# Optimization experiments

Measured on AMD Instinct MI355X. Metric: run time of the kernel, lower is better.

Reference implementation:

```python
import jax, jax.numpy as jnp
import numpy as np

NUM_HEADS = 12
WINDOW = 14  # window size == input_size[0]; rel pos tables are (2*WINDOW-1, head_dim)


def setup_inputs() -> dict:
    key = jax.random.key(0)
    ks = jax.random.split(key, 6)
    C = 768
    x = jax.random.normal(ks[0], (16, 56, 56, C), dtype=jnp.float32)
    qkv_w = jax.random.normal(ks[1], (3 * C, C), dtype=jnp.float32) * 0.02
    qkv_b = jnp.zeros((3 * C,), dtype=jnp.float32)
    proj_w = jax.random.normal(ks[2], (C, C), dtype=jnp.float32) * 0.02
    proj_b = jnp.zeros((C,), dtype=jnp.float32)
    hd = C // NUM_HEADS
    rel_pos_h = jax.random.normal(ks[3], (2 * WINDOW - 1, hd), dtype=jnp.float32) * 0.02
    rel_pos_w = jax.random.normal(ks[4], (2 * WINDOW - 1, hd), dtype=jnp.float32) * 0.02
    return {"x": x, "qkv_w": qkv_w, "qkv_b": qkv_b, "proj_w": proj_w,
            "proj_b": proj_b, "rel_pos_h": rel_pos_h, "rel_pos_w": rel_pos_w}


def reference(x, qkv_w, qkv_b, proj_w, proj_b, rel_pos_h, rel_pos_w):
    B, H, W, C = x.shape
    nh, ws = NUM_HEADS, WINDOW
    hd = C // nh
    scale = hd ** -0.5
    # --- window_partition (H, W divisible by ws -> no padding branch) ---
    xw = x.reshape(B, H // ws, ws, W // ws, ws, C)
    xw = xw.transpose(0, 1, 3, 2, 4, 5).reshape(-1, ws * ws, C)  # (Bw, N, C)
    Bw, N, _ = xw.shape
    # --- qkv projection ---
    qkv = xw @ qkv_w.T + qkv_b  # (Bw, N, 3C)
    qkv = qkv.reshape(Bw, N, 3, nh, hd).transpose(2, 0, 3, 1, 4)
    qkv = qkv.reshape(3, Bw * nh, N, hd)
    q, k, v = qkv[0], qkv[1], qkv[2]
    # --- scaled attention scores ---
    attn = jnp.einsum('bqd,bkd->bqk', q * scale, k)  # (Bw*nh, N, N)
    # --- decomposed relative position bias (q_size == k_size == ws) ---
    idx = jnp.arange(ws)[:, None] - jnp.arange(ws)[None, :] + (ws - 1)
    Rh = rel_pos_h[idx]  # (ws, ws, hd)
    Rw = rel_pos_w[idx]  # (ws, ws, hd)
    rq = q.reshape(Bw * nh, ws, ws, hd)
    rel_h = jnp.einsum('bhwc,hkc->bhwk', rq, Rh)
    rel_w = jnp.einsum('bhwc,wkc->bhwk', rq, Rw)
    attn = (attn.reshape(Bw * nh, ws, ws, ws, ws)
            + rel_h[:, :, :, :, None] + rel_w[:, :, :, None, :])
    attn = jax.nn.softmax(attn.reshape(Bw * nh, N, N), axis=-1)
    # --- weighted values + output projection ---
    out = jnp.einsum('bqk,bkd->bqd', attn, v)
    out = out.reshape(Bw, nh, ws, ws, hd).transpose(0, 2, 3, 1, 4).reshape(Bw, ws, ws, C)
    out = out @ proj_w.T + proj_b
    # --- window_unpartition ---
    out = out.reshape(B, H // ws, W // ws, ws, ws, C)
    out = out.transpose(0, 1, 3, 2, 4, 5).reshape(B, H, W, C)
    return out
```

## Files before the change

kernel.cpp:

```cpp
#include <hip/hip_runtime.h>
#include <stdint.h>

typedef __bf16 bfv8 __attribute__((ext_vector_type(8)));
typedef short s16x8 __attribute__((ext_vector_type(8)));
typedef short s16x4 __attribute__((ext_vector_type(4)));
typedef float f32x4 __attribute__((ext_vector_type(4)));
typedef float f32x16 __attribute__((ext_vector_type(16)));

#define MFMA(a, b, c) __builtin_amdgcn_mfma_f32_16x16x32_bf16(a, b, c, 0, 0, 0)
#define MFMA32(a, b, c) __builtin_amdgcn_mfma_f32_32x32x16_bf16(a, b, c, 0, 0, 0)

__device__ __forceinline__ short f2bf(float f) {
  union { float f; unsigned u; } v; v.f = f;
  unsigned r = v.u + 0x7FFFu + ((v.u >> 16) & 1u);
  return (short)(r >> 16);
}
__device__ __forceinline__ float bf2f(short s) {
  union { unsigned u; float f; } v; v.u = ((unsigned)(unsigned short)s) << 16;
  return v.f;
}
__device__ __forceinline__ unsigned pack2(float a, float b) {
  return (unsigned)(unsigned short)f2bf(a) | ((unsigned)(unsigned short)f2bf(b) << 16);
}
__device__ __forceinline__ bfv8 mkfrag(unsigned a, unsigned b, unsigned c, unsigned d) {
  union { unsigned u[4]; bfv8 v; } t; t.u[0] = a; t.u[1] = b; t.u[2] = c; t.u[3] = d;
  return t.v;
}

__device__ __forceinline__ void async_cp16(const short* g, short* l) {
  auto gp = reinterpret_cast<const uint32_t __attribute__((address_space(1)))*>(
      reinterpret_cast<uintptr_t>(g));
  auto lp = reinterpret_cast<uint32_t __attribute__((address_space(3)))*>(
      reinterpret_cast<uintptr_t>(l));
  __builtin_amdgcn_global_load_lds(gp, lp, 16, 0, 0);
}

__global__ __launch_bounds__(256) void convert_all(
    const float* __restrict__ x, const float* __restrict__ qkvw,
    const float* __restrict__ projw, const float* __restrict__ rph,
    const float* __restrict__ rpw, short* __restrict__ Xbf,
    short* __restrict__ Wq, short* __restrict__ Wp, short* __restrict__ Rhb,
    short* __restrict__ Rwb) {
  const int NX = 9633792;
  const int NW1 = 442368;
  const int NW2 = 147456;
  const int NR = 512;
  int idx = blockIdx.x * 256 + threadIdx.x;
  if (idx < NX) {
    int t = idx / 192, cq = idx - t * 192;
    int wdx = t / 196, n = t - wdx * 196;
    int b = wdx >> 4, wl = wdx & 15;
    int nh = n / 14;
    int hh = (wl >> 2) * 14 + nh;
    int ww = (wl & 3) * 14 + (n - nh * 14);
    float4 v = *(const float4*)(x + ((b * 56 + hh) * 56 + ww) * 768 + cq * 4);
    s16x4 s = {f2bf(v.x), f2bf(v.y), f2bf(v.z), f2bf(v.w)};
    *(s16x4*)(Xbf + idx * 4) = s;
  } else if (idx < NX + NW1) {
    int i = idx - NX;
    float4 v = ((const float4*)qkvw)[i];
    s16x4 s = {f2bf(v.x), f2bf(v.y), f2bf(v.z), f2bf(v.w)};
    *(s16x4*)(Wq + i * 4) = s;
  } else if (idx < NX + NW1 + NW2) {
    int i = idx - NX - NW1;
    float4 v = ((const float4*)projw)[i];
    s16x4 s = {f2bf(v.x), f2bf(v.y), f2bf(v.z), f2bf(v.w)};
    *(s16x4*)(Wp + i * 4) = s;
  } else if (idx < NX + NW1 + NW2 + 2 * NR) {
    int i = idx - NX - NW1 - NW2;
    int which = i >> 9;
    int j = i & 511;
    int p = j >> 4, q = j & 15;
    const float* src = which ? rpw : rph;
    short* dst = which ? Rwb : Rhb;
    s16x4 s = {0, 0, 0, 0};
    if (p < 27) {
      float4 v = *(const float4*)(src + p * 64 + q * 4);
      s = (s16x4){f2bf(v.x), f2bf(v.y), f2bf(v.z), f2bf(v.w)};
    }
    *(s16x4*)(dst + p * 64 + q * 4) = s;
  }
}


#define RPRE(ABASE, BBASE)                                                    \
  const int tid = threadIdx.x, lane = tid & 63, w = tid >> 6;                 \
  const int wr = w >> 2, wc = w & 3;                                          \
  const int li = lane & 15, g = lane >> 4;                                    \
  f32x4 acc[8][4];                                                            \
  _Pragma("unroll") for (int i = 0; i < 8; ++i)                               \
  _Pragma("unroll") for (int j = 0; j < 4; ++j)                               \
      acc[i][j] = (f32x4){0.f, 0.f, 0.f, 0.f};                                \
  const int srow = tid >> 2;                                                  \
  const int schunk = (lane & 3) ^ ((lane >> 3) & 3);                          \
  const short* Asrc0 = (ABASE) + (size_t)(bm * 256 + srow) * 768 + schunk * 8;\
  const short* Asrc1 = Asrc0 + 128 * 768;                                     \
  const short* Bsrc0 = (BBASE) + (size_t)(bn * 256 + srow) * 768 + schunk * 8;\
  const short* Bsrc1 = Bsrc0 + 128 * 768;                                     \
  int aoff[2][4], boff[4];                                                    \
  _Pragma("unroll") for (int mh = 0; mh < 2; ++mh)                            \
  _Pragma("unroll") for (int mf = 0; mf < 4; ++mf) {                          \
    int row = wr * 128 + mh * 64 + mf * 16 + li;                              \
    aoff[mh][mf] = row * 64 + ((g ^ ((row >> 1) & 3)) << 4);                  \
  }                                                                           \
  _Pragma("unroll") for (int nf = 0; nf < 4; ++nf) {                          \
    int row = wc * 64 + nf * 16 + li;                                         \
    boff[nf] = 16384 + row * 64 + ((g ^ ((row >> 1) & 3)) << 4);              \
  }

#define RSTAGE(buf, t)                                                        \
  {                                                                           \
    short* lb = LDSB + (buf) * 16384 + w * 512;                               \
    async_cp16(Asrc0 + (t) * 32, lb);                                         \
    async_cp16(Asrc1 + (t) * 32, lb + 4096);                                  \
    async_cp16(Bsrc0 + (t) * 32, lb + 8192);                                  \
    async_cp16(Bsrc1 + (t) * 32, lb + 12288);                                 \
  }

#define RCOMPUTE(buf)                                                         \
  {                                                                           \
    const char* bb = (const char*)LDSB + (buf) * 32768;                       \
    bfv8 bfr[4];                                                              \
    _Pragma("unroll") for (int nf = 0; nf < 4; ++nf)                          \
        bfr[nf] = *(const bfv8*)(bb + boff[nf]);                              \
    _Pragma("unroll") for (int mh = 0; mh < 2; ++mh) {                        \
      bfv8 af[4];                                                             \
      _Pragma("unroll") for (int mf = 0; mf < 4; ++mf)                        \
          af[mf] = *(const bfv8*)(bb + aoff[mh][mf]);                         \
      __builtin_amdgcn_s_setprio(1);                                          \
      _Pragma("unroll") for (int mf = 0; mf < 4; ++mf)                        \
      _Pragma("unroll") for (int nf = 0; nf < 4; ++nf)                        \
          acc[mh * 4 + mf][nf] = MFMA(af[mf], bfr[nf], acc[mh * 4 + mf][nf]); \
      __builtin_amdgcn_s_setprio(0);                                          \
    }                                                                         \
  }

#define RTILE(buf, t, DOSTAGE, VM)                                            \
  asm volatile("s_waitcnt vmcnt(" VM ")" ::: "memory");                       \
  __builtin_amdgcn_sched_barrier(0);                                          \
  __builtin_amdgcn_s_barrier();                                               \
  __builtin_amdgcn_sched_barrier(0);                                          \
  if (DOSTAGE) { RSTAGE((buf + 2) & 3, (t) + 2); }                            \
  RCOMPUTE(buf);

#define RLOOP()                                                               \
  RSTAGE(0, 0);                                                               \
  RSTAGE(1, 1);                                                               \
  _Pragma("unroll 1") for (int t4 = 0; t4 < 5; ++t4) {                        \
    int tb = t4 * 4;                                                          \
    RTILE(0, tb + 0, true, "4");                                              \
    RTILE(1, tb + 1, true, "4");                                              \
    RTILE(2, tb + 2, true, "4");                                              \
    RTILE(3, tb + 3, true, "4");                                              \
  }                                                                           \
  RTILE(0, 20, true, "4");                                                    \
  RTILE(1, 21, true, "4");                                                    \
  RTILE(2, 22, false, "4");                                                   \
  RTILE(3, 23, false, "0");

__global__ __launch_bounds__(512, 2) void qkv_gemm(
    const short* __restrict__ Xbf, const short* __restrict__ Wq,
    const float* __restrict__ qkvb, short* __restrict__ Q,
    short* __restrict__ K, short* __restrict__ V) {
  __shared__ short LDSB[65536];
  int bid = blockIdx.x;
  int xcd = bid & 7, pos = bid >> 3;
  int wgid = (xcd < 4) ? xcd * 221 + pos : 884 + (xcd - 4) * 220 + pos;
  int bm = wgid / 9, bn = wgid - bm * 9;

  RPRE(Xbf, Wq);
  RLOOP();

  short* dst = (bn < 3) ? Q : ((bn < 6) ? K : V);
  const int head = (bn % 3) * 4 + wc;
  float bias[4];
#pragma unroll
  for (int nf = 0; nf < 4; ++nf) bias[nf] = qkvb[bn * 256 + wc * 64 + nf * 16 + li];
#pragma unroll
  for (int mi = 0; mi < 8; ++mi) {
    int rbase = bm * 256 + wr * 128 + (mi >> 2) * 64 + (mi & 3) * 16 + g * 4;
#pragma unroll
    for (int j = 0; j < 4; ++j) {
      int trow = rbase + j;
      int wdx = trow / 196, n = trow - wdx * 196;
      int base = ((wdx * 12 + head) * 196 + n) * 64;
#pragma unroll
      for (int nf = 0; nf < 4; ++nf)
        dst[base + nf * 16 + li] = f2bf(acc[mi][nf][j] + bias[nf]);
    }
  }
}

__global__ __launch_bounds__(512, 2) void proj_gemm(
    const short* __restrict__ AO, const short* __restrict__ Wp,
    const float* __restrict__ projb, float* __restrict__ out) {
  __shared__ short LDSB[65536];
  int bid = blockIdx.x;
  int xcd = bid & 7, pos = bid >> 3;
  int wgid = (xcd < 4) ? xcd * 74 + pos : 296 + (xcd - 4) * 73 + pos;
  int bm = wgid / 3, bn = wgid - bm * 3;

  RPRE(AO, Wp);
  RLOOP();

  float bias[4];
#pragma unroll
  for (int nf = 0; nf < 4; ++nf) bias[nf] = projb[bn * 256 + wc * 64 + nf * 16 + li];
  const int col0 = bn * 256 + wc * 64 + li;
#pragma unroll
  for (int mi = 0; mi < 8; ++mi) {
    int rbase = bm * 256 + wr * 128 + (mi >> 2) * 64 + (mi & 3) * 16 + g * 4;
#pragma unroll
    for (int j = 0; j < 4; ++j) {
      int trow = rbase + j;
      int wdx = trow / 196, n = trow - wdx * 196;
      int b = wdx >> 4, wl = wdx & 15;
      int nh = n / 14;
      int hh = (wl >> 2) * 14 + nh;
      int ww = (wl & 3) * 14 + (n - nh * 14);
      float* orow = out + ((b * 56 + hh) * 56 + ww) * 768 + col0;
#pragma unroll
      for (int nf = 0; nf < 4; ++nf)
        orow[nf * 16] = acc[mi][nf][j] + bias[nf];
    }
  }
}

__global__ __launch_bounds__(512, 4) void attn_kernel(
    const short* __restrict__ Q, const short* __restrict__ K,
    const short* __restrict__ V, const short* __restrict__ Rhb,
    const short* __restrict__ Rwb, short* __restrict__ AO) {
  __shared__ short Ks[196 * 64];
  __shared__ short Vt[64 * 204];
  __shared__ short relh[224 * 28];
  __shared__ short relw[224 * 28];
  __shared__ short2 hw[224];

  const int bh = blockIdx.x;
  const int wdx = bh / 12, head = bh - wdx * 12;
  const int tid = threadIdx.x, lane = tid & 63, wave = tid >> 6;
  const int l31 = lane & 31, hb = lane >> 5;
  const short* Qb = Q + bh * 12544;
  const short* Kb = K + bh * 12544;
  const short* Vb = V + bh * 12544;

  const int m0 = wave * 32;
  const int qv = (m0 + l31 > 195) ? 195 : m0 + l31;

  bfv8 qf[4];
  if (wave < 7) {
    f32x16 ra = {0.f, 0.f, 0.f, 0.f, 0.f, 0.f, 0.f, 0.f,
                 0.f, 0.f, 0.f, 0.f, 0.f, 0.f, 0.f, 0.f};
    f32x16 rw_ = ra;
#pragma unroll
    for (int s = 0; s < 4; ++s) {
      qf[s] = *(const bfv8*)(Qb + qv * 64 + s * 16 + hb * 8);
      ra = MFMA32(*(const bfv8*)(Rhb + l31 * 64 + s * 16 + hb * 8), qf[s], ra);
      rw_ = MFMA32(*(const bfv8*)(Rwb + l31 * 64 + s * 16 + hb * 8), qf[s], rw_);
    }
#pragma unroll
    for (int reg = 0; reg < 16; ++reg) {
      int p = (reg & 3) + 8 * (reg >> 2) + 4 * hb;
      if (!(hb && reg >= 12)) {
        relh[(m0 + l31) * 28 + p] = f2bf(ra[reg]);
        relw[(m0 + l31) * 28 + p] = f2bf(rw_[reg]);
      }
    }
  }

  if (tid < 64) {
    s16x8 z = {0, 0, 0, 0, 0, 0, 0, 0};
    *(s16x8*)&Vt[tid * 204 + 196] = z;
  }
  for (int c = tid; c < 1568; c += 512) {
    int r = c >> 3, cc = c & 7;
    s16x8 v = *(const s16x8*)(Kb + r * 64 + cc * 8);
    *(s16x8*)&Ks[r * 64 + (((cc ^ (r & 7))) << 3)] = v;
  }
  for (int t = tid; t < 784; t += 512) {
    int dseg = t / 98, kp = t - dseg * 98, d0 = dseg * 8;
    s16x8 a = *(const s16x8*)(Vb + (2 * kp) * 64 + d0);
    s16x8 b = *(const s16x8*)(Vb + (2 * kp + 1) * 64 + d0);
#pragma unroll
    for (int i = 0; i < 8; ++i)
      *(short2*)&Vt[(d0 + i) * 204 + 2 * kp] = make_short2(a[i], b[i]);
  }
  if (tid < 224) {
    int kc = (tid > 195) ? 195 : tid;
    int hk = kc / 14, wk = kc - hk * 14;
    hw[tid] = make_short2((short)(13 - hk), (short)(13 - wk));
  }
  __syncthreads();

  if (wave >= 7) return;

  const int hq = qv / 14;
  const int wq = qv - hq * 14;
  const short* relhq = &relh[qv * 28 + hq];
  const short* relwq = &relw[qv * 28 + wq];

  f32x16 oacc0 = {0.f, 0.f, 0.f, 0.f, 0.f, 0.f, 0.f, 0.f,
                  0.f, 0.f, 0.f, 0.f, 0.f, 0.f, 0.f, 0.f};
  f32x16 oacc1 = oacc0;
  float psum = 0.f;

#pragma unroll
  for (int nt = 0; nt < 7; ++nt) {
    int krow = nt * 32 + l31;
    int krc = (krow > 195) ? 195 : krow;
    const int rb = krc * 64, rx = krc & 7;
    f32x16 st = {0.f, 0.f, 0.f, 0.f, 0.f, 0.f, 0.f, 0.f,
                 0.f, 0.f, 0.f, 0.f, 0.f, 0.f, 0.f, 0.f};
#pragma unroll
    for (int s = 0; s < 4; ++s) {
      bfv8 kf = *(const bfv8*)&Ks[rb + (((2 * s + hb) ^ rx) << 3)];
      st = MFMA32(kf, qf[s], st);
    }
    float pv[16];
    float lsum = 0.f;
#pragma unroll
    for (int reg = 0; reg < 16; ++reg) {
      int koff = (reg & 3) + 8 * (reg >> 2) + 4 * hb;
      int k = nt * 32 + koff;
      short2 dxy = hw[k];
      float b = bf2f(relhq[dxy.x]) + bf2f(relwq[dxy.y]);
      float sv = fmaf(st[reg], 0.125f, b);
      float e = __expf(sv);
      if (nt == 6) {
        if (reg >= 4) e = 0.f;
        else if (hb) e = 0.f;
      }
      pv[reg] = e;
      lsum += e;
    }
    psum += lsum;
    unsigned pk[8], xk[8];
#pragma unroll
    for (int i = 0; i < 8; ++i) pk[i] = pack2(pv[2 * i], pv[2 * i + 1]);
#pragma unroll
    for (int i = 0; i < 8; ++i) xk[i] = (unsigned)__shfl_xor((int)pk[i], 32);

    {
      bfv8 pf = mkfrag(hb ? xk[2] : pk[0], hb ? xk[3] : pk[1],
                       hb ? pk[2] : xk[0], hb ? pk[3] : xk[1]);
      int kb = nt * 32 + hb * 8;
      if (nt == 6 && hb) kb = 0;
      oacc0 = MFMA32(pf, *(const bfv8*)&Vt[l31 * 204 + kb], oacc0);
      oacc1 = MFMA32(pf, *(const bfv8*)&Vt[(32 + l31) * 204 + kb], oacc1);
    }
    {
      bfv8 pf = mkfrag(hb ? xk[6] : pk[4], hb ? xk[7] : pk[5],
                       hb ? pk[6] : xk[4], hb ? pk[7] : xk[5]);
      int kb = nt * 32 + 16 + hb * 8;
      if (nt == 6) kb = 0;
      oacc0 = MFMA32(pf, *(const bfv8*)&Vt[l31 * 204 + kb], oacc0);
      oacc1 = MFMA32(pf, *(const bfv8*)&Vt[(32 + l31) * 204 + kb], oacc1);
    }
  }

  float inv = 1.f / (psum + __shfl_xor(psum, 32));
  short* AOr = AO + (wdx * 196) * 768 + head * 64;
#pragma unroll
  for (int reg = 0; reg < 16; ++reg) {
    int qoff = (reg & 3) + 8 * (reg >> 2) + 4 * hb;
    float invr = __shfl(inv, qoff);
    int q = m0 + qoff;
    if (q < 196) {
      AOr[q * 768 + l31] = f2bf(oacc0[reg] * invr);
      AOr[q * 768 + 32 + l31] = f2bf(oacc1[reg] * invr);
    }
  }
}

extern "C" void kernel_launch(void* const* d_in, const int* in_sizes, int n_in,
                              void* d_out, int out_size, void* d_ws, size_t ws_size,
                              hipStream_t stream) {
  const float* x = (const float*)d_in[0];
  const float* qkv_w = (const float*)d_in[1];
  const float* qkv_b = (const float*)d_in[2];
  const float* proj_w = (const float*)d_in[3];
  const float* proj_b = (const float*)d_in[4];
  const float* rph = (const float*)d_in[5];
  const float* rpw = (const float*)d_in[6];
  float* out = (float*)d_out;

  char* ws = (char*)d_ws;
  short* Q  = (short*)(ws);
  short* K  = (short*)(ws + 77070336);
  short* V  = (short*)(ws + 154140672);
  short* AO = (short*)(ws + 231211008);
  short* Wq = (short*)(ws + 308281344);
  short* Wp = (short*)(ws + 311820288);
  short* Xbf = (short*)d_out;
  short* Rhb = (short*)((char*)d_out + 77070336);
  short* Rwb = Rhb + 2048;

  hipLaunchKernelGGL(convert_all, dim3(39940), dim3(256), 0, stream,
                     x, qkv_w, proj_w, rph, rpw, Xbf, Wq, Wp, Rhb, Rwb);
  hipLaunchKernelGGL(qkv_gemm, dim3(1764), dim3(512), 0, stream,
                     Xbf, Wq, qkv_b, Q, K, V);
  hipLaunchKernelGGL(attn_kernel, dim3(3072), dim3(512), 0, stream,
                     Q, K, V, Rhb, Rwb, AO);
  hipLaunchKernelGGL(proj_gemm, dim3(588), dim3(512), 0, stream,
                     AO, Wp, proj_b, out);
}
```

Before: 469.7 us.

## Restructure GEMM mainloop into K=64 double-buffered tiles with phased MFMA barriers

```diff
diff --git a/kernel.cpp b/kernel.cpp
--- a/kernel.cpp
+++ b/kernel.cpp
@@ -83,7 +83,7 @@
 }
 
 
-#define RPRE(ABASE, BBASE)                                                    \
+#define QPRE(ABASE, BBASE)                                                    \
   const int tid = threadIdx.x, lane = tid & 63, w = tid >> 6;                 \
   const int wr = w >> 2, wc = w & 3;                                          \
   const int li = lane & 15, g = lane >> 4;                                    \
@@ -91,72 +91,98 @@
   _Pragma("unroll") for (int i = 0; i < 8; ++i)                               \
   _Pragma("unroll") for (int j = 0; j < 4; ++j)                               \
       acc[i][j] = (f32x4){0.f, 0.f, 0.f, 0.f};                                \
-  const int srow = tid >> 2;                                                  \
-  const int schunk = (lane & 3) ^ ((lane >> 3) & 3);                          \
-  const short* Asrc0 = (ABASE) + (size_t)(bm * 256 + srow) * 768 + schunk * 8;\
-  const short* Asrc1 = Asrc0 + 128 * 768;                                     \
-  const short* Bsrc0 = (BBASE) + (size_t)(bn * 256 + srow) * 768 + schunk * 8;\
-  const short* Bsrc1 = Bsrc0 + 128 * 768;                                     \
+  const int srow = w * 16 + (lane >> 2);                                      \
+  const int schunk = (lane & 3) ^ ((lane >> 2) & 3);                          \
+  const short* Asrc = (ABASE) + (size_t)(bm * 256 + srow) * 768 + schunk * 8; \
+  const short* Bsrc = (BBASE) + (size_t)(bn * 256 + srow) * 768 + schunk * 8; \
   int aoff[2][4], boff[4];                                                    \
   _Pragma("unroll") for (int mh = 0; mh < 2; ++mh)                            \
   _Pragma("unroll") for (int mf = 0; mf < 4; ++mf) {                          \
     int row = wr * 128 + mh * 64 + mf * 16 + li;                              \
-    aoff[mh][mf] = row * 64 + ((g ^ ((row >> 1) & 3)) << 4);                  \
+    aoff[mh][mf] = row * 32 + ((g ^ (li & 3)) * 8);                           \
   }                                                                           \
   _Pragma("unroll") for (int nf = 0; nf < 4; ++nf) {                          \
     int row = wc * 64 + nf * 16 + li;                                         \
-    boff[nf] = 16384 + row * 64 + ((g ^ ((row >> 1) & 3)) << 4);              \
-  }
-
-#define RSTAGE(buf, t)                                                        \
+    boff[nf] = 16384 + row * 32 + ((g ^ (li & 3)) * 8);                       \
+  }
+
+#define STAGE_KH(t, kh)                                                       \
   {                                                                           \
-    short* lb = LDSB + (buf) * 16384 + w * 512;                               \
-    async_cp16(Asrc0 + (t) * 32, lb);                                         \
-    async_cp16(Asrc1 + (t) * 32, lb + 4096);                                  \
-    async_cp16(Bsrc0 + (t) * 32, lb + 8192);                                  \
-    async_cp16(Bsrc1 + (t) * 32, lb + 12288);                                 \
-  }
-
-#define RCOMPUTE(buf)                                                         \
-  {                                                                           \
-    const char* bb = (const char*)LDSB + (buf) * 32768;                       \
-    bfv8 bfr[4];                                                              \
-    _Pragma("unroll") for (int nf = 0; nf < 4; ++nf)                          \
-        bfr[nf] = *(const bfv8*)(bb + boff[nf]);                              \
-    _Pragma("unroll") for (int mh = 0; mh < 2; ++mh) {                        \
-      bfv8 af[4];                                                             \
-      _Pragma("unroll") for (int mf = 0; mf < 4; ++mf)                        \
-          af[mf] = *(const bfv8*)(bb + aoff[mh][mf]);                         \
-      __builtin_amdgcn_s_setprio(1);                                          \
-      _Pragma("unroll") for (int mf = 0; mf < 4; ++mf)                        \
-      _Pragma("unroll") for (int nf = 0; nf < 4; ++nf)                        \
-          acc[mh * 4 + mf][nf] = MFMA(af[mf], bfr[nf], acc[mh * 4 + mf][nf]); \
-      __builtin_amdgcn_s_setprio(0);                                          \
-    }                                                                         \
-  }
-
-#define RTILE(buf, t, DOSTAGE, VM)                                            \
-  asm volatile("s_waitcnt vmcnt(" VM ")" ::: "memory");                       \
+    short* db = LDSB + ((t) & 1) * 32768 + (kh) * 8192 + w * 512;             \
+    const short* as = Asrc + (size_t)(t) * 64 + (kh) * 32;                    \
+    async_cp16(as, db);                                                       \
+    async_cp16(as + 128 * 768, db + 4096);                                    \
+    const short* bs = Bsrc + (size_t)(t) * 64 + (kh) * 32;                    \
+    async_cp16(bs, db + 16384);                                               \
+    async_cp16(bs + 128 * 768, db + 16384 + 4096);                            \
+  }
+
+#define VMW(N)                                                                \
+  __builtin_amdgcn_sched_barrier(0);                                          \
+  asm volatile("s_waitcnt vmcnt(" N ")" ::: "memory");                        \
+  __builtin_amdgcn_sched_barrier(0);
+
+#define BARS()                                                                \
   __builtin_amdgcn_sched_barrier(0);                                          \
   __builtin_amdgcn_s_barrier();                                               \
-  __builtin_amdgcn_sched_barrier(0);                                          \
-  if (DOSTAGE) { RSTAGE((buf + 2) & 3, (t) + 2); }                            \
-  RCOMPUTE(buf);
-
-#define RLOOP()                                                               \
-  RSTAGE(0, 0);                                                               \
-  RSTAGE(1, 1);                                                               \
-  _Pragma("unroll 1") for (int t4 = 0; t4 < 5; ++t4) {                        \
-    int tb = t4 * 4;                                                          \
-    RTILE(0, tb + 0, true, "4");                                              \
-    RTILE(1, tb + 1, true, "4");                                              \
-    RTILE(2, tb + 2, true, "4");                                              \
-    RTILE(3, tb + 3, true, "4");                                              \
+  __builtin_amdgcn_sched_barrier(0);
+
+#define PHASE_MFMA(mh)                                                        \
+  __builtin_amdgcn_s_setprio(1);                                              \
+  _Pragma("unroll") for (int mf = 0; mf < 4; ++mf)                            \
+  _Pragma("unroll") for (int nf = 0; nf < 4; ++nf)                            \
+      acc[(mh) * 4 + mf][nf] = MFMA(af[mf], bfr[nf], acc[(mh) * 4 + mf][nf]); \
+  __builtin_amdgcn_s_setprio(0);
+
+#define QTILE(t, S1, S3, VMe2, VMe4)                                          \
+  {                                                                           \
+    const short* bbuf = (const short*)LDSB + ((t) & 1) * 32768;               \
+    bfv8 bfr[4], af[4];                                                       \
+        \
+    _Pragma("unroll") for (int nf = 0; nf < 4; ++nf)                          \
+        bfr[nf] = *(const bfv8*)&bbuf[boff[nf]];                              \
+    _Pragma("unroll") for (int mf = 0; mf < 4; ++mf)                          \
+        af[mf] = *(const bfv8*)&bbuf[aoff[0][mf]];                            \
+    if (S1) STAGE_KH((t) + 1, 1);                                             \
+    BARS();                                                                   \
+    PHASE_MFMA(0)                                                             \
+    BARS();                                                                   \
+                                                       \
+    _Pragma("unroll") for (int mf = 0; mf < 4; ++mf)                          \
+        af[mf] = *(const bfv8*)&bbuf[aoff[1][mf]];                            \
+    BARS();                                                                   \
+    PHASE_MFMA(1)                                                             \
+    VMW(VMe2);                \
+    BARS();                                                                   \
+                                                       \
+    _Pragma("unroll") for (int nf = 0; nf < 4; ++nf)                          \
+        bfr[nf] = *(const bfv8*)&bbuf[8192 + boff[nf]];                       \
+    _Pragma("unroll") for (int mf = 0; mf < 4; ++mf)                          \
+        af[mf] = *(const bfv8*)&bbuf[8192 + aoff[0][mf]];                     \
+    if (S3) STAGE_KH((t) + 2, 0);                                             \
+    BARS();                                                                   \
+    PHASE_MFMA(0)                                                             \
+    BARS();                                                                   \
+                                                       \
+    _Pragma("unroll") for (int mf = 0; mf < 4; ++mf)                          \
+        af[mf] = *(const bfv8*)&bbuf[8192 + aoff[1][mf]];                     \
+    BARS();                                                                   \
+    PHASE_MFMA(1)                                                             \
+    VMW(VMe4);              \
+    BARS();                                                                   \
+  }
+
+#define QLOOP()                                                               \
+  STAGE_KH(0, 0);                                                             \
+  STAGE_KH(0, 1);                                                             \
+  STAGE_KH(1, 0);                                                             \
+  VMW("8");                                                                   \
+  BARS();                                                                     \
+  _Pragma("unroll 1") for (int t = 0; t < 10; ++t) {                          \
+    QTILE(t, true, true, "8", "8");                                           \
   }                                                                           \
-  RTILE(0, 20, true, "4");                                                    \
-  RTILE(1, 21, true, "4");                                                    \
-  RTILE(2, 22, false, "4");                                                   \
-  RTILE(3, 23, false, "0");
+  QTILE(10, true, false, "8", "4");                                           \
+  QTILE(11, false, false, "0", "0");
 
 __global__ __launch_bounds__(512, 2) void qkv_gemm(
     const short* __restrict__ Xbf, const short* __restrict__ Wq,
@@ -168,8 +194,8 @@
   int wgid = (xcd < 4) ? xcd * 221 + pos : 884 + (xcd - 4) * 220 + pos;
   int bm = wgid / 9, bn = wgid - bm * 9;
 
-  RPRE(Xbf, Wq);
-  RLOOP();
+  QPRE(Xbf, Wq);
+  QLOOP();
 
   short* dst = (bn < 3) ? Q : ((bn < 6) ? K : V);
   const int head = (bn % 3) * 4 + wc;
@@ -200,8 +226,8 @@
   int wgid = (xcd < 4) ? xcd * 74 + pos : 296 + (xcd - 4) * 73 + pos;
   int bm = wgid / 3, bn = wgid - bm * 3;
 
-  RPRE(AO, Wp);
-  RLOOP();
+  QPRE(AO, Wp);
+  QLOOP();
 
   float bias[4];
 #pragma unroll
```

Measured after the change: 498.1 us. +6.0%, slower.
